# Kernel tuning notes

Hardware: AMD Instinct MI355X
Metric: run time of the kernel (lower is better)

Reference implementation:

```python
import jax, jax.numpy as jnp
import numpy as np

D_MODEL = 1024
N_HEADS = 16
D_K = 64

def setup_inputs() -> dict:
    key = jax.random.key(0)
    k0, k1, k2, k3, k4 = jax.random.split(key, 5)
    B, S = 4, 4096
    std = 0.02
    x = jax.random.normal(k0, (B, S, D_MODEL), dtype=jnp.float32)
    # nn.Linear weights are [out, in]; init normal(0, 0.02) as in _init_weights
    W_q = std * jax.random.normal(k1, (N_HEADS * D_K, D_MODEL), dtype=jnp.float32)
    W_k = std * jax.random.normal(k2, (N_HEADS * D_K, D_MODEL), dtype=jnp.float32)
    W_v = std * jax.random.normal(k3, (N_HEADS * D_K, D_MODEL), dtype=jnp.float32)
    W_o = std * jax.random.normal(k4, (D_MODEL, N_HEADS * D_K), dtype=jnp.float32)
    return {"x": x, "W_q": W_q, "W_k": W_k, "W_v": W_v, "W_o": W_o}

def reference(x, W_q, W_k, W_v, W_o):
    B, S, _ = x.shape
    H, Dk = N_HEADS, D_K
    # projections (nn.Linear: x @ W.T), reshape to [B, S, H, Dk]
    q = (x @ W_q.T).reshape(B, S, H, Dk)
    k = (x @ W_k.T).reshape(B, S, H, Dk)
    v = (x @ W_v.T).reshape(B, S, H, Dk)
    scale = 1.0 / jnp.sqrt(jnp.float32(Dk))
    # No softmax between the two matmuls -> reassociate (QK^T)V = Q(K^TV),
    # identical math, O(S*d^2) instead of O(S^2*d).
    kv = jnp.einsum('bshd,bshe->bhde', k, v)          # [B, H, Dk, Dk]
    attn = jnp.einsum('bshd,bhde->bshe', q, kv) * scale  # [B, S, H, Dk]
    out = attn.reshape(B, S, H * Dk) @ W_o.T
    return out
```

## Files before the change

### kernel.cpp

```cpp
#include <hip/hip_runtime.h>
#include <hip/hip_bf16.h>
#include <cstdint>


typedef __bf16 bf16x8 __attribute__((ext_vector_type(8)));
typedef float f32x4 __attribute__((ext_vector_type(4)));
typedef unsigned short ushort_t;

__device__ inline void gld_lds16(const void* g, void* l) {
    __builtin_amdgcn_global_load_lds(
        (const __attribute__((address_space(1))) unsigned int*)g,
        (__attribute__((address_space(3))) unsigned int*)l,
        16, 0, 0);
}

__device__ inline ushort_t f2bf(float f) {
    uint32_t u = __float_as_uint(f);
    uint32_t r = (u + 0x7fffu + ((u >> 16) & 1u)) >> 16;
    return (ushort_t)r;
}
__device__ inline float bf2f(ushort_t u) {
    return __uint_as_float((uint32_t)u << 16);
}

template <typename OutT>
__global__ __launch_bounds__(256, 2)
void gemm_bt(const ushort_t* __restrict__ A, int lda, long strideA,
             const ushort_t* __restrict__ B, int ldb, long strideB,
             OutT* __restrict__ C0, int ldc0, long strideC0,
             OutT* __restrict__ C1, int ldc1, long strideC1, int nsplit,
             int K, int kslices)
{
    __shared__ ushort_t lA[128 * 32];
    __shared__ ushort_t lB[128 * 32];

    const int t    = threadIdx.x;
    const int lane = t & 63;
    const int wid  = t >> 6;

    const int z = blockIdx.z;
    int bb, ks;
    if (kslices == 4) { bb = z >> 2; ks = z & 3; }
    else              { bb = z;      ks = 0;     }

    A += (size_t)bb * strideA + (size_t)ks * K;
    B += (size_t)bb * strideB + (size_t)ks * K;

    const int m0 = blockIdx.x * 128;
    const int n0 = blockIdx.y * 128;

    const int wm = (wid >> 1) * 64;
    const int wn = (wid & 1) * 64;
    const int mr = lane & 15;
    const int q4 = lane >> 4;

    const int row_a = t >> 2;
    const int seg   = ((t & 3) ^ ((t >> 3) & 3)) * 8;
    const int csw   = (q4 ^ ((mr >> 1) & 3)) * 16;

    f32x4 acc[4][4] = {};

    for (int k0 = 0; k0 < K; k0 += 32) {
        __syncthreads();
        gld_lds16(A + (size_t)(m0 + row_a) * lda + k0 + seg,      (char*)lA + wid * 1024);
        gld_lds16(A + (size_t)(m0 + 64 + row_a) * lda + k0 + seg, (char*)lA + 4096 + wid * 1024);
        gld_lds16(B + (size_t)(n0 + row_a) * ldb + k0 + seg,      (char*)lB + wid * 1024);
        gld_lds16(B + (size_t)(n0 + 64 + row_a) * ldb + k0 + seg, (char*)lB + 4096 + wid * 1024);
        __syncthreads();

        bf16x8 af[4], bf[4];
#pragma unroll
        for (int i = 0; i < 4; ++i)
            af[i] = *(const bf16x8*)((const char*)lA + (wm + i * 16 + mr) * 64 + csw);
#pragma unroll
        for (int j = 0; j < 4; ++j)
            bf[j] = *(const bf16x8*)((const char*)lB + (wn + j * 16 + mr) * 64 + csw);
#pragma unroll
        for (int i = 0; i < 4; ++i)
#pragma unroll
            for (int j = 0; j < 4; ++j)
                acc[i][j] = __builtin_amdgcn_mfma_f32_16x16x32_bf16(af[i], bf[j], acc[i][j], 0, 0, 0);
    }

    OutT* Cw; int ldcw, nc0;
    if (n0 < nsplit) { Cw = C0 + (size_t)z * strideC0; ldcw = ldc0; nc0 = n0; }
    else             { Cw = C1 + (size_t)z * strideC1; ldcw = ldc1; nc0 = n0 - nsplit; }

#pragma unroll
    for (int i = 0; i < 4; ++i) {
        const int rbase = m0 + wm + i * 16 + q4 * 4;
#pragma unroll
        for (int j = 0; j < 4; ++j) {
            const int col = nc0 + wn + j * 16 + mr;
#pragma unroll
            for (int r = 0; r < 4; ++r) {
                const float v = acc[i][j][r];
                const size_t off = (size_t)(rbase + r) * ldcw + col;
                if constexpr (sizeof(OutT) == 2) Cw[off] = f2bf(v);
                else                             Cw[off] = v;
            }
        }
    }
}

__global__ __launch_bounds__(256)
void cast_x_t(const float* __restrict__ x, ushort_t* __restrict__ xb,
              ushort_t* __restrict__ xbT)
{
    __shared__ ushort_t lt[64 * 66];
    const int t  = threadIdx.x;
    const int s0 = blockIdx.x * 64;
    const int i0 = blockIdx.y * 64;

#pragma unroll
    for (int c = 0; c < 4; ++c) {
        const int idx = c * 256 + t;
        const int r = idx >> 4, c4 = (idx & 15) * 4;
        const float4 f = *(const float4*)&x[(size_t)(s0 + r) * 1024 + i0 + c4];
        ushort4 o;
        o.x = f2bf(f.x); o.y = f2bf(f.y); o.z = f2bf(f.z); o.w = f2bf(f.w);
        *(ushort4*)&xb[(size_t)(s0 + r) * 1024 + i0 + c4] = o;
        *(uint32_t*)&lt[r * 66 + c4]     = (uint32_t)o.x | ((uint32_t)o.y << 16);
        *(uint32_t*)&lt[r * 66 + c4 + 2] = (uint32_t)o.z | ((uint32_t)o.w << 16);
    }
    __syncthreads();
#pragma unroll
    for (int c = 0; c < 4; ++c) {
        const int idx = c * 256 + t;
        const int ri = idx >> 4, s4 = (idx & 15) * 4;
        ushort4 o;
        o.x = lt[(s4 + 0) * 66 + ri];
        o.y = lt[(s4 + 1) * 66 + ri];
        o.z = lt[(s4 + 2) * 66 + ri];
        o.w = lt[(s4 + 3) * 66 + ri];
        *(ushort4*)&xbT[(size_t)(i0 + ri) * 16384 + s0 + s4] = o;
    }
}

__global__ __launch_bounds__(256)
void cast_wt(const float* __restrict__ W, ushort_t* __restrict__ WT)
{
    __shared__ ushort_t lt[64 * 66];
    const int t  = threadIdx.x;
    const int r0 = blockIdx.x * 64;
    const int c0 = blockIdx.y * 64;

#pragma unroll
    for (int c = 0; c < 4; ++c) {
        const int idx = c * 256 + t;
        const int r = idx >> 4, c4 = (idx & 15) * 4;
        const float4 f = *(const float4*)&W[(size_t)(r0 + r) * 1024 + c0 + c4];
        ushort4 o;
        o.x = f2bf(f.x); o.y = f2bf(f.y); o.z = f2bf(f.z); o.w = f2bf(f.w);
        *(uint32_t*)&lt[r * 66 + c4]     = (uint32_t)o.x | ((uint32_t)o.y << 16);
        *(uint32_t*)&lt[r * 66 + c4 + 2] = (uint32_t)o.z | ((uint32_t)o.w << 16);
    }
    __syncthreads();
#pragma unroll
    for (int c = 0; c < 4; ++c) {
        const int idx = c * 256 + t;
        const int ri = idx >> 4, s4 = (idx & 15) * 4;
        ushort4 o;
        o.x = lt[(s4 + 0) * 66 + ri];
        o.y = lt[(s4 + 1) * 66 + ri];
        o.z = lt[(s4 + 2) * 66 + ri];
        o.w = lt[(s4 + 3) * 66 + ri];
        *(ushort4*)&WT[(size_t)(c0 + ri) * 1024 + r0 + s4] = o;
    }
}

__global__ __launch_bounds__(256)
void cast_w2(const float* __restrict__ a, const float* __restrict__ b,
             ushort_t* __restrict__ out)
{
    const float* src = (blockIdx.y == 0) ? a : b;
    const int i = (blockIdx.x * 256 + threadIdx.x) * 4;
    const float4 f = *(const float4*)&src[i];
    ushort4 o;
    o.x = f2bf(f.x); o.y = f2bf(f.y); o.z = f2bf(f.z); o.w = f2bf(f.w);
    *(ushort4*)&out[(size_t)blockIdx.y * 1048576 + i] = o;
}

__global__ __launch_bounds__(256)
void reduce_g(const ushort4* __restrict__ Gp, ushort4* __restrict__ G)
{
    const int gid = blockIdx.x * 256 + threadIdx.x;
    const int b = gid >> 18, r = gid & 262143;
    float s0 = 0.f, s1 = 0.f, s2 = 0.f, s3 = 0.f;
#pragma unroll
    for (int ks = 0; ks < 4; ++ks) {
        const ushort4 u = Gp[(size_t)(b * 4 + ks) * 262144 + r];
        s0 += bf2f(u.x); s1 += bf2f(u.y); s2 += bf2f(u.z); s3 += bf2f(u.w);
    }
    ushort4 o;
    o.x = f2bf(s0); o.y = f2bf(s1); o.z = f2bf(s2); o.w = f2bf(s3);
    G[gid] = o;
}

__global__ __launch_bounds__(256)
void kvblk(const ushort_t* __restrict__ H, const ushort_t* __restrict__ Wv,
           float* __restrict__ KVp)
{
    __shared__ ushort_t sH[64 * 132];
    __shared__ ushort_t sV[64 * 132];

    const int t  = threadIdx.x;
    const int is = blockIdx.x;
    const int bh = blockIdx.y;
    const int b  = bh >> 4, h = bh & 15;

    const ushort_t* Hp = H + ((size_t)b << 20) + (size_t)(h * 64) * 1024 + is * 128;
    const ushort_t* Vp = Wv + (size_t)(h * 64) * 1024 + is * 128;

#pragma unroll
    for (int i2 = 0; i2 < 8; ++i2) {
        const int ci = i2 * 256 + t;
        const int r = ci >> 5, c = (ci & 31) * 4;
        *(uint2*)&sH[r * 132 + c] = *(const uint2*)&Hp[(size_t)r * 1024 + c];
        *(uint2*)&sV[r * 132 + c] = *(const uint2*)&Vp[(size_t)r * 1024 + c];
    }
    __syncthreads();

    const int d0 = (t >> 4) * 4;
    const int e0 = (t & 15) * 4;
    float acc[4][4] = {};

#pragma unroll 2
    for (int i4 = 0; i4 < 128; i4 += 4) {
        uint2 hu[4], vu[4];
#pragma unroll
        for (int j = 0; j < 4; ++j) {
            hu[j] = *(const uint2*)&sH[(d0 + j) * 132 + i4];
            vu[j] = *(const uint2*)&sV[(e0 + j) * 132 + i4];
        }
        float hf[4][4], vf[4][4];
#pragma unroll
        for (int j = 0; j < 4; ++j) {
            hf[j][0] = __uint_as_float(hu[j].x << 16);
            hf[j][1] = __uint_as_float(hu[j].x & 0xffff0000u);
            hf[j][2] = __uint_as_float(hu[j].y << 16);
            hf[j][3] = __uint_as_float(hu[j].y & 0xffff0000u);
            vf[j][0] = __uint_as_float(vu[j].x << 16);
            vf[j][1] = __uint_as_float(vu[j].x & 0xffff0000u);
            vf[j][2] = __uint_as_float(vu[j].y << 16);
            vf[j][3] = __uint_as_float(vu[j].y & 0xffff0000u);
        }
#pragma unroll
        for (int ii = 0; ii < 4; ++ii)
#pragma unroll
            for (int di = 0; di < 4; ++di)
#pragma unroll
                for (int ej = 0; ej < 4; ++ej)
                    acc[di][ej] += hf[di][ii] * vf[ej][ii];
    }

    float* outp = KVp + ((size_t)(is * 64 + bh)) * 4096;
#pragma unroll
    for (int i = 0; i < 4; ++i) {
        float4 o; o.x = acc[i][0]; o.y = acc[i][1]; o.z = acc[i][2]; o.w = acc[i][3];
        *(float4*)&outp[(d0 + i) * 64 + e0] = o;
    }
}

__global__ __launch_bounds__(256)
void reduce_kv8(const float4* __restrict__ in, float4* __restrict__ out)
{
    const int i = blockIdx.x * 256 + threadIdx.x;
    float4 a = in[i];
#pragma unroll
    for (int s = 1; s < 8; ++s) {
        const float4 b = in[s * 65536 + i];
        a.x += b.x; a.y += b.y; a.z += b.z; a.w += b.w;
    }
    out[i] = a;
}

__global__ __launch_bounds__(256)
void make_E(const float* __restrict__ KV, const float* __restrict__ Wo,
            ushort_t* __restrict__ Et)
{
    __shared__ float skv[64 * 65];
    __shared__ float swo[64 * 65];

    const int t  = threadIdx.x;
    const int bh = blockIdx.y;
    const int b  = bh >> 4, h = bh & 15;
    const int j0 = blockIdx.x * 64;

    const float* kvp = KV + (size_t)bh * 4096;
#pragma unroll
    for (int i = 0; i < 4; ++i) {
        const int idx = t + i * 256;
        const int r = idx >> 4, c = (idx & 15) * 4;
        const float4 f = *(const float4*)&kvp[r * 64 + c];
        skv[r * 65 + c + 0] = f.x;
        skv[r * 65 + c + 1] = f.y;
        skv[r * 65 + c + 2] = f.z;
        skv[r * 65 + c + 3] = f.w;
        const float4 g = *(const float4*)&Wo[(size_t)(j0 + r) * 1024 + h * 64 + c];
        swo[r * 65 + c + 0] = g.x;
        swo[r * 65 + c + 1] = g.y;
        swo[r * 65 + c + 2] = g.z;
        swo[r * 65 + c + 3] = g.w;
    }
    __syncthreads();

    const int d0 = (t & 15) * 4;
#pragma unroll
    for (int pass = 0; pass < 4; ++pass) {
        const int jloc = (t >> 4) + pass * 16;
        float s0 = 0.f, s1 = 0.f, s2 = 0.f, s3 = 0.f;
        const float* wrow = &swo[jloc * 65];
#pragma unroll 8
        for (int e = 0; e < 64; ++e) {
            const float w = wrow[e];
            s0 += skv[(d0 + 0) * 65 + e] * w;
            s1 += skv[(d0 + 1) * 65 + e] * w;
            s2 += skv[(d0 + 2) * 65 + e] * w;
            s3 += skv[(d0 + 3) * 65 + e] * w;
        }
        ushort4 o;
        o.x = f2bf(s0 * 0.125f);
        o.y = f2bf(s1 * 0.125f);
        o.z = f2bf(s2 * 0.125f);
        o.w = f2bf(s3 * 0.125f);
        *(ushort4*)&Et[((size_t)b * 1024 + j0 + jloc) * 1024 + h * 64 + d0] = o;
    }
}


extern "C" void kernel_launch(void* const* d_in, const int* in_sizes, int n_in,
                              void* d_out, int out_size, void* d_ws, size_t ws_size,
                              hipStream_t stream)
{
    const float* x  = (const float*)d_in[0];
    const float* Wq = (const float*)d_in[1];
    const float* Wk = (const float*)d_in[2];
    const float* Wv = (const float*)d_in[3];
    const float* Wo = (const float*)d_in[4];
    float* out = (float*)d_out;

    const int B = 4, S = 4096, D = 1024;
    const long MB1 = 1048576;

    char* ws = (char*)d_ws;
    size_t off = 0;
    auto alloc = [&](size_t bytes) -> void* {
        void* p = ws + off;
        off += (bytes + 255) & ~(size_t)255;
        return p;
    };
    ushort_t* xb   = (ushort_t*)alloc((size_t)B * S * D * 2);
    ushort_t* xbT  = (ushort_t*)alloc((size_t)D * B * S * 2);
    ushort_t* wkv  = (ushort_t*)alloc((size_t)2 * D * D * 2);
    ushort_t* wqT  = (ushort_t*)alloc((size_t)D * D * 2);
    ushort_t* Gb   = (ushort_t*)alloc((size_t)B * D * D * 2);
    float*    kvp  = (float*)alloc((size_t)8 * 64 * 4096 * 4);
    float*    kvr  = (float*)alloc((size_t)64 * 4096 * 4);
    char*     R1   = (char*)alloc((size_t)16 * MB1 * 2);
    ushort_t* Gp = (ushort_t*)R1;
    ushort_t* Hb = (ushort_t*)R1;
    ushort_t* Et = (ushort_t*)(R1 + 8 * MB1 * 2);
    ushort_t* Fb = (ushort_t*)(R1 + 16 * MB1 * 2 - 8 * MB1 * 2);
    ushort_t* wkb = wkv;
    ushort_t* wvb = wkv + MB1;

    cast_x_t<<<dim3(256, 16), dim3(256), 0, stream>>>(x, xb, xbT);
    cast_w2<<<dim3(1024, 2), dim3(256), 0, stream>>>(Wk, Wv, wkv);
    cast_wt<<<dim3(16, 16), dim3(256), 0, stream>>>(Wq, wqT);

    gemm_bt<ushort_t><<<dim3(8, 8, 16), dim3(256), 0, stream>>>(
        xbT, 16384, 4096, xbT, 16384, 4096,
        Gp, D, MB1, (ushort_t*)nullptr, 0, 0, 1 << 30, D, 4);
    reduce_g<<<dim3(4096), dim3(256), 0, stream>>>((const ushort4*)Gp, (ushort4*)Gb);

    gemm_bt<ushort_t><<<dim3(8, 8, 4), dim3(256), 0, stream>>>(
        wkb, D, 0, Gb, D, MB1,
        Hb, D, MB1, (ushort_t*)nullptr, 0, 0, 1 << 30, D, 1);

    kvblk<<<dim3(8, 64), dim3(256), 0, stream>>>(Hb, wvb, kvp);
    reduce_kv8<<<dim3(256), dim3(256), 0, stream>>>((const float4*)kvp, (float4*)kvr);

    make_E<<<dim3(16, 64), dim3(256), 0, stream>>>(kvr, Wo, Et);

    gemm_bt<ushort_t><<<dim3(8, 8, 4), dim3(256), 0, stream>>>(
        Et, D, MB1, wqT, D, 0,
        Fb, D, MB1, (ushort_t*)nullptr, 0, 0, 1 << 30, D, 1);

    gemm_bt<float><<<dim3(32, 8, 4), dim3(256), 0, stream>>>(
        xb, D, (long)S * D, Fb, D, MB1,
        out, D, (long)S * D, (float*)nullptr, 0, 0, 1 << 30, D, 1);
}
```

Before: 339.5 us.

## Exploit Gram matrix symmetry: compute upper-triangle tiles and mirror during reduction

```diff
diff --git a/kernel.cpp b/kernel.cpp
--- a/kernel.cpp
+++ b/kernel.cpp
@@ -27,9 +27,7 @@
 __global__ __launch_bounds__(256, 2)
 void gemm_bt(const ushort_t* __restrict__ A, int lda, long strideA,
              const ushort_t* __restrict__ B, int ldb, long strideB,
-             OutT* __restrict__ C0, int ldc0, long strideC0,
-             OutT* __restrict__ C1, int ldc1, long strideC1, int nsplit,
-             int K, int kslices)
+             OutT* __restrict__ C0, int ldc0, long strideC0, int K)
 {
     __shared__ ushort_t lA[128 * 32];
     __shared__ ushort_t lB[128 * 32];
@@ -37,14 +35,10 @@
     const int t    = threadIdx.x;
     const int lane = t & 63;
     const int wid  = t >> 6;
-
-    const int z = blockIdx.z;
-    int bb, ks;
-    if (kslices == 4) { bb = z >> 2; ks = z & 3; }
-    else              { bb = z;      ks = 0;     }
-
-    A += (size_t)bb * strideA + (size_t)ks * K;
-    B += (size_t)bb * strideB + (size_t)ks * K;
+    const int z    = blockIdx.z;
+
+    A += (size_t)z * strideA;
+    B += (size_t)z * strideB;
 
     const int m0 = blockIdx.x * 128;
     const int n0 = blockIdx.y * 128;
@@ -82,24 +76,141 @@
                 acc[i][j] = __builtin_amdgcn_mfma_f32_16x16x32_bf16(af[i], bf[j], acc[i][j], 0, 0, 0);
     }
 
-    OutT* Cw; int ldcw, nc0;
-    if (n0 < nsplit) { Cw = C0 + (size_t)z * strideC0; ldcw = ldc0; nc0 = n0; }
-    else             { Cw = C1 + (size_t)z * strideC1; ldcw = ldc1; nc0 = n0 - nsplit; }
-
+    OutT* Cw = C0 + (size_t)z * strideC0;
 #pragma unroll
     for (int i = 0; i < 4; ++i) {
         const int rbase = m0 + wm + i * 16 + q4 * 4;
 #pragma unroll
         for (int j = 0; j < 4; ++j) {
-            const int col = nc0 + wn + j * 16 + mr;
+            const int col = n0 + wn + j * 16 + mr;
 #pragma unroll
             for (int r = 0; r < 4; ++r) {
                 const float v = acc[i][j][r];
-                const size_t off = (size_t)(rbase + r) * ldcw + col;
+                const size_t off = (size_t)(rbase + r) * ldc0 + col;
                 if constexpr (sizeof(OutT) == 2) Cw[off] = f2bf(v);
                 else                             Cw[off] = v;
             }
         }
+    }
+}
+
+__global__ __launch_bounds__(256, 2)
+void gemm_gram(const ushort_t* __restrict__ X, ushort_t* __restrict__ Gp)
+{
+    __shared__ ushort_t lA[128 * 32];
+    __shared__ ushort_t lB[128 * 32];
+
+    const int t    = threadIdx.x;
+    const int lane = t & 63;
+    const int wid  = t >> 6;
+
+    const int z  = blockIdx.x;
+    const int bb = z >> 2, ks = z & 3;
+
+    int ti = 0, rem = blockIdx.y;
+    while (rem >= 8 - ti) { rem -= 8 - ti; ++ti; }
+    const int tj = ti + rem;
+    const int m0 = ti * 128;
+    const int n0 = tj * 128;
+
+    const ushort_t* A = X + (size_t)bb * 4096 + (size_t)ks * 1024;
+
+    const int wm = (wid >> 1) * 64;
+    const int wn = (wid & 1) * 64;
+    const int mr = lane & 15;
+    const int q4 = lane >> 4;
+
+    const int row_a = t >> 2;
+    const int seg   = ((t & 3) ^ ((t >> 3) & 3)) * 8;
+    const int csw   = (q4 ^ ((mr >> 1) & 3)) * 16;
+
+    f32x4 acc[4][4] = {};
+
+    for (int k0 = 0; k0 < 1024; k0 += 32) {
+        __syncthreads();
+        gld_lds16(A + (size_t)(m0 + row_a) * 16384 + k0 + seg,      (char*)lA + wid * 1024);
+        gld_lds16(A + (size_t)(m0 + 64 + row_a) * 16384 + k0 + seg, (char*)lA + 4096 + wid * 1024);
+        gld_lds16(A + (size_t)(n0 + row_a) * 16384 + k0 + seg,      (char*)lB + wid * 1024);
+        gld_lds16(A + (size_t)(n0 + 64 + row_a) * 16384 + k0 + seg, (char*)lB + 4096 + wid * 1024);
+        __syncthreads();
+
+        bf16x8 af[4], bf[4];
+#pragma unroll
+        for (int i = 0; i < 4; ++i)
+            af[i] = *(const bf16x8*)((const char*)lA + (wm + i * 16 + mr) * 64 + csw);
+#pragma unroll
+        for (int j = 0; j < 4; ++j)
+            bf[j] = *(const bf16x8*)((const char*)lB + (wn + j * 16 + mr) * 64 + csw);
+#pragma unroll
+        for (int i = 0; i < 4; ++i)
+#pragma unroll
+            for (int j = 0; j < 4; ++j)
+                acc[i][j] = __builtin_amdgcn_mfma_f32_16x16x32_bf16(af[i], bf[j], acc[i][j], 0, 0, 0);
+    }
+
+    ushort_t* Cw = Gp + ((size_t)z << 20);
+#pragma unroll
+    for (int i = 0; i < 4; ++i) {
+        const int rbase = m0 + wm + i * 16 + q4 * 4;
+#pragma unroll
+        for (int j = 0; j < 4; ++j) {
+            const int col = n0 + wn + j * 16 + mr;
+#pragma unroll
+            for (int r = 0; r < 4; ++r)
+                Cw[(size_t)(rbase + r) * 1024 + col] = f2bf(acc[i][j][r]);
+        }
+    }
+}
+
+__global__ __launch_bounds__(256)
+void reduce_g_t(const ushort_t* __restrict__ Gp, ushort_t* __restrict__ G)
+{
+    __shared__ float acc[64 * 65];
+
+    const int t  = threadIdx.x;
+    const int b  = blockIdx.y;
+    const int tr = blockIdx.x >> 4, tc = blockIdx.x & 15;
+    const int sr = (tr <= tc) ? tr : tc;
+    const int sc = (tr <= tc) ? tc : tr;
+    const bool flip = tr > tc;
+
+#pragma unroll
+    for (int p = 0; p < 4; ++p) {
+        const int idx = p * 256 + t;
+        const int r = idx >> 4, c = (idx & 15) * 4;
+        float a0 = 0.f, a1 = 0.f, a2 = 0.f, a3 = 0.f;
+#pragma unroll
+        for (int ksl = 0; ksl < 4; ++ksl) {
+            const ushort4 u = *(const ushort4*)&Gp[((size_t)(b * 4 + ksl) << 20)
+                                                   + (size_t)(sr * 64 + r) * 1024 + sc * 64 + c];
+            a0 += bf2f(u.x); a1 += bf2f(u.y); a2 += bf2f(u.z); a3 += bf2f(u.w);
+        }
+        acc[r * 65 + c + 0] = a0;
+        acc[r * 65 + c + 1] = a1;
+        acc[r * 65 + c + 2] = a2;
+        acc[r * 65 + c + 3] = a3;
+    }
+    __syncthreads();
+
+#pragma unroll
+    for (int p = 0; p < 4; ++p) {
+        const int idx = p * 256 + t;
+        const int r = idx >> 4, c = (idx & 15) * 4;
+        float v0, v1, v2, v3;
+        if (flip) {
+            v0 = acc[(c + 0) * 65 + r];
+            v1 = acc[(c + 1) * 65 + r];
+            v2 = acc[(c + 2) * 65 + r];
+            v3 = acc[(c + 3) * 65 + r];
+        } else {
+            v0 = acc[r * 65 + c + 0];
+            v1 = acc[r * 65 + c + 1];
+            v2 = acc[r * 65 + c + 2];
+            v3 = acc[r * 65 + c + 3];
+        }
+        ushort4 o;
+        o.x = f2bf(v0); o.y = f2bf(v1); o.z = f2bf(v2); o.w = f2bf(v3);
+        *(ushort4*)&G[((size_t)b << 20) + (size_t)(tr * 64 + r) * 1024 + tc * 64 + c] = o;
     }
 }
 
@@ -179,22 +290,6 @@
     ushort4 o;
     o.x = f2bf(f.x); o.y = f2bf(f.y); o.z = f2bf(f.z); o.w = f2bf(f.w);
     *(ushort4*)&out[(size_t)blockIdx.y * 1048576 + i] = o;
-}
-
-__global__ __launch_bounds__(256)
-void reduce_g(const ushort4* __restrict__ Gp, ushort4* __restrict__ G)
-{
-    const int gid = blockIdx.x * 256 + threadIdx.x;
-    const int b = gid >> 18, r = gid & 262143;
-    float s0 = 0.f, s1 = 0.f, s2 = 0.f, s3 = 0.f;
-#pragma unroll
-    for (int ks = 0; ks < 4; ++ks) {
-        const ushort4 u = Gp[(size_t)(b * 4 + ks) * 262144 + r];
-        s0 += bf2f(u.x); s1 += bf2f(u.y); s2 += bf2f(u.z); s3 += bf2f(u.w);
-    }
-    ushort4 o;
-    o.x = f2bf(s0); o.y = f2bf(s1); o.z = f2bf(s2); o.w = f2bf(s3);
-    G[gid] = o;
 }
 
 __global__ __launch_bounds__(256)
@@ -357,11 +452,11 @@
     ushort_t* Gb   = (ushort_t*)alloc((size_t)B * D * D * 2);
     float*    kvp  = (float*)alloc((size_t)8 * 64 * 4096 * 4);
     float*    kvr  = (float*)alloc((size_t)64 * 4096 * 4);
+    ushort_t* Fb   = (ushort_t*)alloc((size_t)B * D * D * 2);
     char*     R1   = (char*)alloc((size_t)16 * MB1 * 2);
     ushort_t* Gp = (ushort_t*)R1;
     ushort_t* Hb = (ushort_t*)R1;
     ushort_t* Et = (ushort_t*)(R1 + 8 * MB1 * 2);
-    ushort_t* Fb = (ushort_t*)(R1 + 16 * MB1 * 2 - 8 * MB1 * 2);
     ushort_t* wkb = wkv;
     ushort_t* wvb = wkv + MB1;
 
@@ -369,14 +464,11 @@
     cast_w2<<<dim3(1024, 2), dim3(256), 0, stream>>>(Wk, Wv, wkv);
     cast_wt<<<dim3(16, 16), dim3(256), 0, stream>>>(Wq, wqT);
 
-    gemm_bt<ushort_t><<<dim3(8, 8, 16), dim3(256), 0, stream>>>(
-        xbT, 16384, 4096, xbT, 16384, 4096,
-        Gp, D, MB1, (ushort_t*)nullptr, 0, 0, 1 << 30, D, 4);
-    reduce_g<<<dim3(4096), dim3(256), 0, stream>>>((const ushort4*)Gp, (ushort4*)Gb);
+    gemm_gram<<<dim3(16, 36), dim3(256), 0, stream>>>(xbT, Gp);
+    reduce_g_t<<<dim3(256, 4), dim3(256), 0, stream>>>(Gp, Gb);
 
     gemm_bt<ushort_t><<<dim3(8, 8, 4), dim3(256), 0, stream>>>(
-        wkb, D, 0, Gb, D, MB1,
-        Hb, D, MB1, (ushort_t*)nullptr, 0, 0, 1 << 30, D, 1);
+        wkb, D, 0, Gb, D, MB1, Hb, D, MB1, D);
 
     kvblk<<<dim3(8, 64), dim3(256), 0, stream>>>(Hb, wvb, kvp);
     reduce_kv8<<<dim3(256), dim3(256), 0, stream>>>((const float4*)kvp, (float4*)kvr);
@@ -384,10 +476,8 @@
     make_E<<<dim3(16, 64), dim3(256), 0, stream>>>(kvr, Wo, Et);
 
     gemm_bt<ushort_t><<<dim3(8, 8, 4), dim3(256), 0, stream>>>(
-        Et, D, MB1, wqT, D, 0,
-        Fb, D, MB1, (ushort_t*)nullptr, 0, 0, 1 << 30, D, 1);
+        Et, D, MB1, wqT, D, 0, Fb, D, (long)D * D, D);
 
     gemm_bt<float><<<dim3(32, 8, 4), dim3(256), 0, stream>>>(
-        xb, D, (long)S * D, Fb, D, MB1,
-        out, D, (long)S * D, (float*)nullptr, 0, 0, 1 << 30, D, 1);
-}
+        xb, D, (long)S * D, Fb, D, (long)D * D, out, D, (long)S * D, D);
+}
```

After: 315.6 us. 1.08x faster.
